# Optimization experiments

Hardware: AMD Instinct MI355X
Metric: run time of the kernel (lower is better)

The kernel has to match this reference:

```python
import jax, jax.numpy as jnp
import numpy as np

N_NODES = 100000

def gcn_conv(x, W, b, row, col, n_nodes):
    """PyG-style GCNConv: add self-loops, symmetric deg normalization,
    linear transform, scatter-add aggregation over edges, plus bias."""
    h = x @ W  # [N, out]
    loop = jnp.arange(n_nodes, dtype=row.dtype)
    r = jnp.concatenate([row, loop])  # source nodes
    c = jnp.concatenate([col, loop])  # target nodes
    w = jnp.ones(r.shape[0], dtype=x.dtype)  # edge_weight=None -> ones (incl. self-loop fill=1)
    deg = jax.ops.segment_sum(w, c, num_segments=n_nodes)
    dinv = jnp.where(deg > 0, jax.lax.rsqrt(deg), 0.0).astype(x.dtype)
    norm = dinv[r] * dinv[c]  # [E+N]
    msg = h[r] * norm[:, None]  # gather + scale, [E+N, out]
    out = jax.ops.segment_sum(msg, c, num_segments=n_nodes)
    return out + b


def setup_inputs() -> dict:
    key = jax.random.key(0)
    k0, k1, k2, k3, k4, k5 = jax.random.split(key, 6)
    F_in, H, C = 128, 64, 40
    E = 1_600_000
    x = jax.random.normal(k0, (N_NODES, F_in), dtype=jnp.float32)
    edge_index = jax.random.randint(k1, (2, E), 0, N_NODES, dtype=jnp.int64 if jax.config.jax_enable_x64 else jnp.int32)
    # Glorot init like torch Linear
    s1 = 1.0 / np.sqrt(F_in)
    s2 = 1.0 / np.sqrt(H)
    W1 = jax.random.uniform(k2, (F_in, H), jnp.float32, -s1, s1)
    b1 = jax.random.uniform(k3, (H,), jnp.float32, -s1, s1)
    W2 = jax.random.uniform(k4, (H, C), jnp.float32, -s2, s2)
    b2 = jax.random.uniform(k5, (C,), jnp.float32, -s2, s2)
    return {"x": x, "edge_index": edge_index, "W1": W1, "b1": b1, "W2": W2, "b2": b2}


def reference(x, edge_index, W1, b1, W2, b2):
    row, col = edge_index[0], edge_index[1]
    # eval mode: dropout(p=0.5, training=False) is identity
    h = gcn_conv(x, W1, b1, row, col, N_NODES)
    h = jax.nn.relu(h)
    out = gcn_conv(h, W2, b2, row, col, N_NODES)
    return out
```

## Files before the change

kernel.cpp:

```cpp
#include <hip/hip_runtime.h>
#include <hip/hip_fp16.h>


#define FIN 128
#define H1  64
#define C2  40
#define GP  64
#define TILE 8192
#define BCAP 6144

__global__ __launch_bounds__(256) void k_hist(const int* __restrict__ col, int E,
                                              int* __restrict__ bucketCnt, int NB) {
    __shared__ int lh[512];
    int t = threadIdx.x;
    for (int i = t; i < NB; i += 256) lh[i] = 0;
    __syncthreads();
    int base = blockIdx.x * TILE;
    int cnt = min(TILE, E - base);
    for (int i = t; i < cnt; i += 256) atomicAdd(&lh[col[base + i] >> 8], 1);
    __syncthreads();
    for (int b = t; b < NB; b += 256) if (lh[b]) atomicAdd(&bucketCnt[b], lh[b]);
}

__global__ __launch_bounds__(512) void k_scan(const int* __restrict__ bucketCnt,
                                              int* __restrict__ rawBase,
                                              int* __restrict__ padBase,
                                              int* __restrict__ gcursor,
                                              __half* __restrict__ h1,
                                              __half* __restrict__ g,
                                              int NB, int N) {
    __shared__ int sr[512], sp[512];
    int t = threadIdx.x;
    int c = (t < NB) ? bucketCnt[t] : 0;
    int p = (t < NB) ? (((c + 3) & ~3) + 1024) : 0;
    sr[t] = c; sp[t] = p;
    __syncthreads();
    for (int off = 1; off < 512; off <<= 1) {
        int a = (t >= off) ? sr[t - off] : 0;
        int b = (t >= off) ? sp[t - off] : 0;
        __syncthreads();
        sr[t] += a; sp[t] += b;
        __syncthreads();
    }
    if (t <= NB) {
        rawBase[t] = sr[t] - ((t < NB) ? c : 0);
        padBase[t] = sp[t] - ((t < NB) ? p : 0);
        if (t < NB) gcursor[t] = sr[t] - c;
    }
    if (t < 32) ((unsigned*)(h1 + (size_t)N * H1))[t] = 0u;
    else if (t < 64) ((unsigned*)(g + (size_t)N * GP))[t - 32] = 0u;
}

__global__ __launch_bounds__(512) void k_scatter(const int* __restrict__ row,
                                                 const int* __restrict__ col,
                                                 int* __restrict__ gcursor,
                                                 int* __restrict__ pairs,
                                                 int E, int NB) {
    __shared__ int2 stage[TILE];
    __shared__ int lcnt[512];
    __shared__ int lex[512];
    __shared__ int gbase[512];
    int t = threadIdx.x, tile = blockIdx.x;
    int base = tile * TILE;
    int cnt = min(TILE, E - base);

    lcnt[t] = 0;
    __syncthreads();
    for (int i = t; i < cnt; i += 512) atomicAdd(&lcnt[col[base + i] >> 8], 1);
    __syncthreads();

    int myc = lcnt[t];
    lex[t] = myc;
    __syncthreads();
    for (int off = 1; off < 512; off <<= 1) {
        int u = (t >= off) ? lex[t - off] : 0;
        __syncthreads();
        lex[t] += u;
        __syncthreads();
    }
    int ex = lex[t] - myc;
    __syncthreads();
    lex[t] = ex;
    lcnt[t] = ex;
    if (t < NB && myc > 0) gbase[t] = atomicAdd(&gcursor[t], myc);
    __syncthreads();

    for (int i = t; i < cnt; i += 512) {
        int r = row[base + i], c = col[base + i];
        int lpos = atomicAdd(&lcnt[c >> 8], 1);
        stage[lpos] = make_int2(r, c);
    }
    __syncthreads();

    for (int i = t; i < cnt; i += 512) {
        int2 p = stage[i];
        int b = p.y >> 8;
        pairs[gbase[b] + (i - lex[b])] = p.x | ((p.y & 255) << 24);
    }
}

__global__ __launch_bounds__(512) void k_bucket(const int* __restrict__ pairs,
                                                const int* __restrict__ rawBase,
                                                const int* __restrict__ padBase,
                                                int* __restrict__ rowptr,
                                                int* __restrict__ deg,
                                                int* __restrict__ esrc,
                                                int N, int NB) {
    __shared__ int dcnt[256];
    __shared__ int sr[256], sp[256];
    __shared__ int cur[256];
    __shared__ int outbuf[BCAP];
    int t = threadIdx.x, b = blockIdx.x;
    int d0 = b << 8;
    int nd = min(256, N - d0);
    int bstart = rawBase[b];
    int cnt = rawBase[b + 1] - bstart;
    int pstart = padBase[b];

    if (t < 256) dcnt[t] = 0;
    __syncthreads();
    for (int i = t; i < cnt; i += 512) {
        unsigned p = (unsigned)pairs[bstart + i];
        atomicAdd(&dcnt[p >> 24], 1);
    }
    __syncthreads();

    int myc = 0, myp = 0;
    if (t < 256) {
        myc = dcnt[t];
        myp = (myc + 3) & ~3;
        sr[t] = myc; sp[t] = myp;
    }
    __syncthreads();
    for (int off = 1; off < 256; off <<= 1) {
        int a = 0, c2 = 0;
        if (t < 256 && t >= off) { a = sr[t - off]; c2 = sp[t - off]; }
        __syncthreads();
        if (t < 256) { sr[t] += a; sp[t] += c2; }
        __syncthreads();
    }
    if (t < 256) {
        int pex = sp[t] - myp;
        cur[t] = pex;
        if (t < nd) {
            rowptr[d0 + t] = pstart + pex;
            deg[d0 + t] = myc;
        }
    }
    __syncthreads();
    int pcnt = sp[255];

    if (pcnt <= BCAP) {
        for (int i = t; i < cnt; i += 512) {
            unsigned p = (unsigned)pairs[bstart + i];
            int lpos = atomicAdd(&cur[p >> 24], 1);
            outbuf[lpos] = (int)(p & 0xFFFFFF);
        }
        __syncthreads();
        if (t < 256) {
            int pex = sp[t] - myp;
            for (int j = myc; j < myp; ++j) outbuf[pex + j] = N;
        }
        __syncthreads();
        for (int i = t; i < pcnt; i += 512) esrc[pstart + i] = outbuf[i];
    } else {
        for (int i = t; i < cnt; i += 512) {
            unsigned p = (unsigned)pairs[bstart + i];
            int lpos = atomicAdd(&cur[p >> 24], 1);
            esrc[pstart + lpos] = (int)(p & 0xFFFFFF);
        }
        __syncthreads();
        if (t < 256) {
            int pex = sp[t] - myp;
            for (int j = myc; j < myp; ++j) esrc[pstart + pex + j] = N;
        }
    }
}

__global__ __launch_bounds__(256) void k_gemm1(const float* __restrict__ x,
                                               const float* __restrict__ W1,
                                               const int* __restrict__ deg,
                                               __half* __restrict__ h1, int N) {
    __shared__ float smem[FIN * H1 + 64 * (FIN + 4)];
    __shared__ float sdc[64];
    int t = threadIdx.x;
    float* Ws = smem;
    float (*xs)[FIN + 4] = (float (*)[FIN + 4])(smem + FIN * H1);
    int node0 = blockIdx.x * 64;

    const float4* W4 = (const float4*)W1;
    float4* Ws4 = (float4*)Ws;
#pragma unroll
    for (int j = 0; j < 8; ++j) Ws4[t + j * 256] = W4[t + j * 256];

    const float4* x4 = (const float4*)x;
#pragma unroll
    for (int j = 0; j < 8; ++j) {
        int idx = t + j * 256;
        int r = idx >> 5, kq = idx & 31;
        int node = node0 + r; if (node >= N) node = N - 1;
        float4 v = x4[(size_t)node * 32 + kq];
        *(float4*)&xs[r][kq * 4] = v;
    }
    if (t < 64) {
        int node = node0 + t;
        sdc[t] = (node < N) ? rsqrtf((float)deg[node] + 1.0f) : 0.f;
    }
    __syncthreads();

    int og = t & 15, ng = t >> 4;
    int o0 = og * 4, n0 = ng * 4;
    float acc[4][4];
#pragma unroll
    for (int i = 0; i < 4; ++i)
#pragma unroll
        for (int j = 0; j < 4; ++j) acc[i][j] = 0.f;

#pragma unroll 8
    for (int k = 0; k < FIN; ++k) {
        float a0 = xs[n0 + 0][k], a1 = xs[n0 + 1][k];
        float a2 = xs[n0 + 2][k], a3 = xs[n0 + 3][k];
        float4 w = *(const float4*)&Ws[k * H1 + o0];
        acc[0][0] += a0 * w.x; acc[0][1] += a0 * w.y; acc[0][2] += a0 * w.z; acc[0][3] += a0 * w.w;
        acc[1][0] += a1 * w.x; acc[1][1] += a1 * w.y; acc[1][2] += a1 * w.z; acc[1][3] += a1 * w.w;
        acc[2][0] += a2 * w.x; acc[2][1] += a2 * w.y; acc[2][2] += a2 * w.z; acc[2][3] += a2 * w.w;
        acc[3][0] += a3 * w.x; acc[3][1] += a3 * w.y; acc[3][2] += a3 * w.z; acc[3][3] += a3 * w.w;
    }

#pragma unroll
    for (int i = 0; i < 4; ++i) {
        int node = node0 + n0 + i;
        if (node < N) {
            float dcv = sdc[n0 + i];
            union { __half h[4]; uint2 u; } pk;
            pk.h[0] = __float2half_rn(acc[i][0] * dcv);
            pk.h[1] = __float2half_rn(acc[i][1] * dcv);
            pk.h[2] = __float2half_rn(acc[i][2] * dcv);
            pk.h[3] = __float2half_rn(acc[i][3] * dcv);
            *(uint2*)&h1[(size_t)node * H1 + o0] = pk.u;
        }
    }
}

__global__ __launch_bounds__(512) void k_agg1mm(const int* __restrict__ rowptr,
                                                const int* __restrict__ deg,
                                                const int* __restrict__ esrc,
                                                const __half* __restrict__ h1,
                                                const float* __restrict__ b1,
                                                const float* __restrict__ W2,
                                                __half* __restrict__ g, int N) {
    __shared__ float hs[64][H1 + 4];
    __shared__ float Ws[H1 * C2];
    __shared__ float sdc[64];
    int t = threadIdx.x;
    int node0 = blockIdx.x * 64;

    {
        const float4* W4 = (const float4*)W2;
        float4* Ws4 = (float4*)Ws;
        for (int i = t; i < 640; i += 512) Ws4[i] = W4[i];
    }

    int wv = t >> 6, lane = t & 63;
    int half = lane >> 5;
    int f = lane & 31;
    float2 b1v = *(const float2*)&b1[2 * f];
    const __half2* hp = (const __half2*)h1;

    for (int j = 0; j < 8; ++j) {
        int r = wv * 8 + j;
        int node = node0 + r;
        if (node >= N) {
            if (lane < 32) { hs[r][2 * f] = 0.f; hs[r][2 * f + 1] = 0.f; }
            if (lane == 0) sdc[r] = 0.f;
            continue;
        }
        int start = rowptr[node], d = deg[node];
        int d4 = (d + 3) & ~3;
        float dc = rsqrtf((float)d + 1.0f);
        float ax = 0.f, ay = 0.f;
        int i = 0;
        for (; i + 8 <= d4; i += 8) {
            int4 s = *(const int4*)&esrc[start + i + half * 4];
            float2 v0 = __half22float2(hp[s.x * 32 + f]);
            float2 v1 = __half22float2(hp[s.y * 32 + f]);
            float2 v2 = __half22float2(hp[s.z * 32 + f]);
            float2 v3 = __half22float2(hp[s.w * 32 + f]);
            ax += (v0.x + v1.x) + (v2.x + v3.x);
            ay += (v0.y + v1.y) + (v2.y + v3.y);
        }
        if (i < d4 && half == 0) {
            int4 s = *(const int4*)&esrc[start + i];
            float2 v0 = __half22float2(hp[s.x * 32 + f]);
            float2 v1 = __half22float2(hp[s.y * 32 + f]);
            float2 v2 = __half22float2(hp[s.z * 32 + f]);
            float2 v3 = __half22float2(hp[s.w * 32 + f]);
            ax += (v0.x + v1.x) + (v2.x + v3.x);
            ay += (v0.y + v1.y) + (v2.y + v3.y);
        }
        ax += __shfl(ax, lane ^ 32);
        ay += __shfl(ay, lane ^ 32);
        float2 sv = __half22float2(hp[node * 32 + f]);
        ax = fmaxf(fmaf(dc, ax + sv.x, b1v.x), 0.f);
        ay = fmaxf(fmaf(dc, ay + sv.y, b1v.y), 0.f);
        if (lane < 32) { hs[r][2 * f] = ax; hs[r][2 * f + 1] = ay; }
        if (lane == 0) sdc[r] = dc;
    }
    __syncthreads();

    int og = t & 15, ng = t >> 4;
    int o0 = og * 4, n0 = ng * 2;
    int o0c = (o0 <= 36) ? o0 : 36;
    float acc[2][4];
#pragma unroll
    for (int i = 0; i < 2; ++i)
#pragma unroll
        for (int j = 0; j < 4; ++j) acc[i][j] = 0.f;

#pragma unroll 8
    for (int k = 0; k < H1; ++k) {
        float a0 = hs[n0 + 0][k], a1 = hs[n0 + 1][k];
        float4 w = *(const float4*)&Ws[k * C2 + o0c];
        acc[0][0] += a0 * w.x; acc[0][1] += a0 * w.y; acc[0][2] += a0 * w.z; acc[0][3] += a0 * w.w;
        acc[1][0] += a1 * w.x; acc[1][1] += a1 * w.y; acc[1][2] += a1 * w.z; acc[1][3] += a1 * w.w;
    }

    if (o0 < C2) {
#pragma unroll
        for (int i = 0; i < 2; ++i) {
            int node = node0 + n0 + i;
            if (node < N) {
                float dcv = sdc[n0 + i];
                union { __half h[4]; uint2 u; } pk;
                pk.h[0] = __float2half_rn(acc[i][0] * dcv);
                pk.h[1] = __float2half_rn(acc[i][1] * dcv);
                pk.h[2] = __float2half_rn(acc[i][2] * dcv);
                pk.h[3] = __float2half_rn(acc[i][3] * dcv);
                *(uint2*)&g[(size_t)node * GP + o0] = pk.u;
            }
        }
    }
}

__global__ __launch_bounds__(256) void k_agg2(const int* __restrict__ rowptr,
                                              const int* __restrict__ deg,
                                              const int* __restrict__ esrc,
                                              const __half* __restrict__ g,
                                              const float* __restrict__ b2,
                                              float* __restrict__ out, int N) {
    int w = (int)((blockIdx.x * blockDim.x + threadIdx.x) >> 6);
    int lane = threadIdx.x & 63;
    if (w >= N) return;
    int half = lane >> 5;
    int f = lane & 31;
    bool act = f < 20;
    const __half2* gp = (const __half2*)g;

    int start = rowptr[w], d = deg[w];
    int d4 = (d + 3) & ~3;
    float dc = rsqrtf((float)d + 1.0f);
    float ax = 0.f, ay = 0.f;
    int i = 0;
    for (; i + 8 <= d4; i += 8) {
        int4 s = *(const int4*)&esrc[start + i + half * 4];
        float2 v0 = __half22float2(gp[s.x * 32 + f]);
        float2 v1 = __half22float2(gp[s.y * 32 + f]);
        float2 v2 = __half22float2(gp[s.z * 32 + f]);
        float2 v3 = __half22float2(gp[s.w * 32 + f]);
        ax += (v0.x + v1.x) + (v2.x + v3.x);
        ay += (v0.y + v1.y) + (v2.y + v3.y);
    }
    if (i < d4 && half == 0) {
        int4 s = *(const int4*)&esrc[start + i];
        float2 v0 = __half22float2(gp[s.x * 32 + f]);
        float2 v1 = __half22float2(gp[s.y * 32 + f]);
        float2 v2 = __half22float2(gp[s.z * 32 + f]);
        float2 v3 = __half22float2(gp[s.w * 32 + f]);
        ax += (v0.x + v1.x) + (v2.x + v3.x);
        ay += (v0.y + v1.y) + (v2.y + v3.y);
    }
    ax += __shfl(ax, lane ^ 32);
    ay += __shfl(ay, lane ^ 32);
    if (lane < 32 && act) {
        float2 b2v = *(const float2*)&b2[2 * f];
        float2 sv = __half22float2(gp[w * 32 + f]);
        float2 o;
        o.x = fmaf(dc, ax + sv.x, b2v.x);
        o.y = fmaf(dc, ay + sv.y, b2v.y);
        *(float2*)&out[(size_t)w * C2 + 2 * f] = o;
    }
}

extern "C" void kernel_launch(void* const* d_in, const int* in_sizes, int n_in,
                              void* d_out, int out_size, void* d_ws, size_t ws_size,
                              hipStream_t stream) {
    const float* x   = (const float*)d_in[0];
    const int*   ei  = (const int*)d_in[1];
    const float* W1  = (const float*)d_in[2];
    const float* b1  = (const float*)d_in[3];
    const float* W2  = (const float*)d_in[4];
    const float* b2  = (const float*)d_in[5];
    float* out = (float*)d_out;

    const int N = in_sizes[0] / FIN;
    const int E = in_sizes[1] / 2;
    const int* row = ei;
    const int* col = ei + E;

    const int NB = (N + 255) >> 8;
    const int T  = (E + TILE - 1) / TILE;
    const int EP = E + NB * 1024 + 1024;

    char* ws = (char*)d_ws;
    size_t off = 0;
    int*    bucketCnt = (int*)(ws + off);    off += (size_t)NB * 4;
    int*    rawBase   = (int*)(ws + off);    off += (size_t)(NB + 1) * 4;
    int*    padBase   = (int*)(ws + off);    off += (size_t)(NB + 1) * 4;
    int*    gcursor   = (int*)(ws + off);    off += (size_t)NB * 4;
    int*    deg       = (int*)(ws + off);    off += (size_t)N * 4;
    int*    rowptr    = (int*)(ws + off);    off += (size_t)N * 4;
    int*    pairs     = (int*)(ws + off);    off += (size_t)E * 4;
    off = (off + 15) & ~(size_t)15;
    int*    esrc      = (int*)(ws + off);    off += (size_t)EP * 4;
    off = (off + 15) & ~(size_t)15;
    __half* h1        = (__half*)(ws + off); off += (size_t)(N + 1) * H1 * 2;
    off = (off + 15) & ~(size_t)15;
    __half* g         = (__half*)(ws + off); off += (size_t)(N + 1) * GP * 2;

    hipMemsetAsync(bucketCnt, 0, (size_t)NB * 4, stream);

    int gblocks = (N + 63) / 64;

    k_hist<<<T, 256, 0, stream>>>(col, E, bucketCnt, NB);
    k_scan<<<1, 512, 0, stream>>>(bucketCnt, rawBase, padBase, gcursor, h1, g, NB, N);
    k_scatter<<<T, 512, 0, stream>>>(row, col, gcursor, pairs, E, NB);
    k_bucket<<<NB, 512, 0, stream>>>(pairs, rawBase, padBase, rowptr, deg, esrc, N, NB);

    k_gemm1<<<gblocks, 256, 0, stream>>>(x, W1, deg, h1, N);

    k_agg1mm<<<gblocks, 512, 0, stream>>>(rowptr, deg, esrc, h1, b1, W2, g, N);

    k_agg2<<<((size_t)N * 64 + 255) / 256, 256, 0, stream>>>(rowptr, deg, esrc, g, b2, out, N);
}
```

Measured before the change: 260.4 us.

## Use split-fp16 MFMA for first GEMM and widen gather unroll to eight

The first linear layer moves from scalar FP32 FMAs to MFMA 16x16x16 fp16 instructions. Both x and a transposed W1 are split into hi/lo fp16 parts, and three MFMAs per tile keep accuracy close to FP32. The W1 split is precomputed in the scan kernel. CSR padding goes from 4 to 8 and both aggregation kernels gather eight neighbours per half-wave per iteration to raise memory-level parallelism, at the cost of more padding entries. The second GEMM reads activations as float4, and BCAP is increased.

```diff
diff --git a/kernel.cpp b/kernel.cpp
--- a/kernel.cpp
+++ b/kernel.cpp
@@ -7,7 +7,11 @@
 #define C2  40
 #define GP  64
 #define TILE 8192
-#define BCAP 6144
+#define BCAP 7168
+#define WTS 132
+
+typedef _Float16 half4_t __attribute__((ext_vector_type(4)));
+typedef float float4_t __attribute__((ext_vector_type(4)));
 
 __global__ __launch_bounds__(256) void k_hist(const int* __restrict__ col, int E,
                                               int* __restrict__ bucketCnt, int NB) {
@@ -28,11 +32,14 @@
                                               int* __restrict__ gcursor,
                                               __half* __restrict__ h1,
                                               __half* __restrict__ g,
+                                              const float* __restrict__ W1,
+                                              _Float16* __restrict__ W1th,
+                                              _Float16* __restrict__ W1tl,
                                               int NB, int N) {
     __shared__ int sr[512], sp[512];
     int t = threadIdx.x;
     int c = (t < NB) ? bucketCnt[t] : 0;
-    int p = (t < NB) ? (((c + 3) & ~3) + 1024) : 0;
+    int p = (t < NB) ? (((c + 7) & ~7) + 2048) : 0;
     sr[t] = c; sp[t] = p;
     __syncthreads();
     for (int off = 1; off < 512; off <<= 1) {
@@ -49,6 +56,13 @@
     }
     if (t < 32) ((unsigned*)(h1 + (size_t)N * H1))[t] = 0u;
     else if (t < 64) ((unsigned*)(g + (size_t)N * GP))[t - 32] = 0u;
+    for (int i = t; i < FIN * H1; i += 512) {
+        int o = i >> 7, k = i & 127;
+        float wv = W1[k * H1 + o];
+        _Float16 hi = (_Float16)wv;
+        W1th[o * WTS + k] = hi;
+        W1tl[o * WTS + k] = (_Float16)(wv - (float)hi);
+    }
 }
 
 __global__ __launch_bounds__(512) void k_scatter(const int* __restrict__ row,
@@ -128,7 +142,7 @@
     int myc = 0, myp = 0;
     if (t < 256) {
         myc = dcnt[t];
-        myp = (myc + 3) & ~3;
+        myp = (myc + 7) & ~7;
         sr[t] = myc; sp[t] = myp;
     }
     __syncthreads();
@@ -177,67 +191,68 @@
     }
 }
 
-__global__ __launch_bounds__(256) void k_gemm1(const float* __restrict__ x,
-                                               const float* __restrict__ W1,
-                                               const int* __restrict__ deg,
-                                               __half* __restrict__ h1, int N) {
-    __shared__ float smem[FIN * H1 + 64 * (FIN + 4)];
-    __shared__ float sdc[64];
+__global__ __launch_bounds__(256) void k_gemm1m(const float* __restrict__ x,
+                                                const _Float16* __restrict__ W1th,
+                                                const _Float16* __restrict__ W1tl,
+                                                const int* __restrict__ deg,
+                                                __half* __restrict__ h1, int N) {
+    __shared__ alignas(16) _Float16 Wh[H1 * WTS];
+    __shared__ alignas(16) _Float16 Wl[H1 * WTS];
     int t = threadIdx.x;
-    float* Ws = smem;
-    float (*xs)[FIN + 4] = (float (*)[FIN + 4])(smem + FIN * H1);
-    int node0 = blockIdx.x * 64;
-
-    const float4* W4 = (const float4*)W1;
-    float4* Ws4 = (float4*)Ws;
-#pragma unroll
-    for (int j = 0; j < 8; ++j) Ws4[t + j * 256] = W4[t + j * 256];
-
-    const float4* x4 = (const float4*)x;
-#pragma unroll
-    for (int j = 0; j < 8; ++j) {
-        int idx = t + j * 256;
-        int r = idx >> 5, kq = idx & 31;
-        int node = node0 + r; if (node >= N) node = N - 1;
-        float4 v = x4[(size_t)node * 32 + kq];
-        *(float4*)&xs[r][kq * 4] = v;
-    }
-    if (t < 64) {
-        int node = node0 + t;
-        sdc[t] = (node < N) ? rsqrtf((float)deg[node] + 1.0f) : 0.f;
-    }
-    __syncthreads();
-
-    int og = t & 15, ng = t >> 4;
-    int o0 = og * 4, n0 = ng * 4;
-    float acc[4][4];
-#pragma unroll
-    for (int i = 0; i < 4; ++i)
-#pragma unroll
-        for (int j = 0; j < 4; ++j) acc[i][j] = 0.f;
-
-#pragma unroll 8
-    for (int k = 0; k < FIN; ++k) {
-        float a0 = xs[n0 + 0][k], a1 = xs[n0 + 1][k];
-        float a2 = xs[n0 + 2][k], a3 = xs[n0 + 3][k];
-        float4 w = *(const float4*)&Ws[k * H1 + o0];
-        acc[0][0] += a0 * w.x; acc[0][1] += a0 * w.y; acc[0][2] += a0 * w.z; acc[0][3] += a0 * w.w;
-        acc[1][0] += a1 * w.x; acc[1][1] += a1 * w.y; acc[1][2] += a1 * w.z; acc[1][3] += a1 * w.w;
-        acc[2][0] += a2 * w.x; acc[2][1] += a2 * w.y; acc[2][2] += a2 * w.z; acc[2][3] += a2 * w.w;
-        acc[3][0] += a3 * w.x; acc[3][1] += a3 * w.y; acc[3][2] += a3 * w.z; acc[3][3] += a3 * w.w;
-    }
-
-#pragma unroll
-    for (int i = 0; i < 4; ++i) {
-        int node = node0 + n0 + i;
-        if (node < N) {
-            float dcv = sdc[n0 + i];
+
+    {
+        const uint4* sh = (const uint4*)W1th;
+        const uint4* sl = (const uint4*)W1tl;
+        uint4* dh = (uint4*)Wh;
+        uint4* dl = (uint4*)Wl;
+        for (int i = t; i < (H1 * WTS) / 8; i += 256) { dh[i] = sh[i]; dl[i] = sl[i]; }
+    }
+
+    int wv = t >> 6, l = t & 63;
+    int col = l & 15;
+    int krow = l >> 4;
+    int node = blockIdx.x * 64 + wv * 16 + col;
+    int nodec = min(node, N - 1);
+
+    half4_t bh[8], bl[8];
+    const float4* xr = (const float4*)(x + (size_t)nodec * FIN);
+#pragma unroll
+    for (int kt = 0; kt < 8; ++kt) {
+        float4 v = xr[kt * 4 + krow];
+        half4_t hi, lo;
+        hi[0] = (_Float16)v.x; lo[0] = (_Float16)(v.x - (float)hi[0]);
+        hi[1] = (_Float16)v.y; lo[1] = (_Float16)(v.y - (float)hi[1]);
+        hi[2] = (_Float16)v.z; lo[2] = (_Float16)(v.z - (float)hi[2]);
+        hi[3] = (_Float16)v.w; lo[3] = (_Float16)(v.w - (float)hi[3]);
+        bh[kt] = hi; bl[kt] = lo;
+    }
+    float dcv = rsqrtf((float)deg[nodec] + 1.0f);
+    __syncthreads();
+
+    float4_t acc[4];
+#pragma unroll
+    for (int ot = 0; ot < 4; ++ot) acc[ot] = (float4_t){0.f, 0.f, 0.f, 0.f};
+
+#pragma unroll
+    for (int kt = 0; kt < 8; ++kt) {
+#pragma unroll
+        for (int ot = 0; ot < 4; ++ot) {
+            int aoff = ((ot * 16 + col) * WTS + kt * 16 + krow * 4) >> 2;
+            half4_t ah = ((const half4_t*)Wh)[aoff];
+            half4_t al = ((const half4_t*)Wl)[aoff];
+            acc[ot] = __builtin_amdgcn_mfma_f32_16x16x16f16(ah, bh[kt], acc[ot], 0, 0, 0);
+            acc[ot] = __builtin_amdgcn_mfma_f32_16x16x16f16(ah, bl[kt], acc[ot], 0, 0, 0);
+            acc[ot] = __builtin_amdgcn_mfma_f32_16x16x16f16(al, bh[kt], acc[ot], 0, 0, 0);
+        }
+    }
+
+    if (node < N) {
+#pragma unroll
+        for (int ot = 0; ot < 4; ++ot) {
             union { __half h[4]; uint2 u; } pk;
-            pk.h[0] = __float2half_rn(acc[i][0] * dcv);
-            pk.h[1] = __float2half_rn(acc[i][1] * dcv);
-            pk.h[2] = __float2half_rn(acc[i][2] * dcv);
-            pk.h[3] = __float2half_rn(acc[i][3] * dcv);
-            *(uint2*)&h1[(size_t)node * H1 + o0] = pk.u;
+#pragma unroll
+            for (int r = 0; r < 4; ++r) pk.h[r] = __float2half_rn(acc[ot][r] * dcv);
+            *(uint2*)&h1[(size_t)node * H1 + ot * 16 + krow * 4] = pk.u;
         }
     }
 }
@@ -276,11 +291,26 @@
             continue;
         }
         int start = rowptr[node], d = deg[node];
-        int d4 = (d + 3) & ~3;
+        int d8 = (d + 7) & ~7;
         float dc = rsqrtf((float)d + 1.0f);
         float ax = 0.f, ay = 0.f;
         int i = 0;
-        for (; i + 8 <= d4; i += 8) {
+        for (; i + 16 <= d8; i += 16) {
+            int b0 = start + i + half * 8;
+            int4 sA = *(const int4*)&esrc[b0];
+            int4 sB = *(const int4*)&esrc[b0 + 4];
+            float2 v0 = __half22float2(hp[sA.x * 32 + f]);
+            float2 v1 = __half22float2(hp[sA.y * 32 + f]);
+            float2 v2 = __half22float2(hp[sA.z * 32 + f]);
+            float2 v3 = __half22float2(hp[sA.w * 32 + f]);
+            float2 v4 = __half22float2(hp[sB.x * 32 + f]);
+            float2 v5 = __half22float2(hp[sB.y * 32 + f]);
+            float2 v6 = __half22float2(hp[sB.z * 32 + f]);
+            float2 v7 = __half22float2(hp[sB.w * 32 + f]);
+            ax += ((v0.x + v1.x) + (v2.x + v3.x)) + ((v4.x + v5.x) + (v6.x + v7.x));
+            ay += ((v0.y + v1.y) + (v2.y + v3.y)) + ((v4.y + v5.y) + (v6.y + v7.y));
+        }
+        if (i < d8) {
             int4 s = *(const int4*)&esrc[start + i + half * 4];
             float2 v0 = __half22float2(hp[s.x * 32 + f]);
             float2 v1 = __half22float2(hp[s.y * 32 + f]);
@@ -289,15 +319,6 @@
             ax += (v0.x + v1.x) + (v2.x + v3.x);
             ay += (v0.y + v1.y) + (v2.y + v3.y);
         }
-        if (i < d4 && half == 0) {
-            int4 s = *(const int4*)&esrc[start + i];
-            float2 v0 = __half22float2(hp[s.x * 32 + f]);
-            float2 v1 = __half22float2(hp[s.y * 32 + f]);
-            float2 v2 = __half22float2(hp[s.z * 32 + f]);
-            float2 v3 = __half22float2(hp[s.w * 32 + f]);
-            ax += (v0.x + v1.x) + (v2.x + v3.x);
-            ay += (v0.y + v1.y) + (v2.y + v3.y);
-        }
         ax += __shfl(ax, lane ^ 32);
         ay += __shfl(ay, lane ^ 32);
         float2 sv = __half22float2(hp[node * 32 + f]);
@@ -317,12 +338,20 @@
 #pragma unroll
         for (int j = 0; j < 4; ++j) acc[i][j] = 0.f;
 
-#pragma unroll 8
-    for (int k = 0; k < H1; ++k) {
-        float a0 = hs[n0 + 0][k], a1 = hs[n0 + 1][k];
-        float4 w = *(const float4*)&Ws[k * C2 + o0c];
-        acc[0][0] += a0 * w.x; acc[0][1] += a0 * w.y; acc[0][2] += a0 * w.z; acc[0][3] += a0 * w.w;
-        acc[1][0] += a1 * w.x; acc[1][1] += a1 * w.y; acc[1][2] += a1 * w.z; acc[1][3] += a1 * w.w;
+#pragma unroll
+    for (int k = 0; k < H1; k += 4) {
+        float4 a0 = *(const float4*)&hs[n0 + 0][k];
+        float4 a1 = *(const float4*)&hs[n0 + 1][k];
+        float ar0[4] = {a0.x, a0.y, a0.z, a0.w};
+        float ar1[4] = {a1.x, a1.y, a1.z, a1.w};
+#pragma unroll
+        for (int kk = 0; kk < 4; ++kk) {
+            float4 w = *(const float4*)&Ws[(k + kk) * C2 + o0c];
+            acc[0][0] += ar0[kk] * w.x; acc[0][1] += ar0[kk] * w.y;
+            acc[0][2] += ar0[kk] * w.z; acc[0][3] += ar0[kk] * w.w;
+            acc[1][0] += ar1[kk] * w.x; acc[1][1] += ar1[kk] * w.y;
+            acc[1][2] += ar1[kk] * w.z; acc[1][3] += ar1[kk] * w.w;
+        }
     }
 
     if (o0 < C2) {
@@ -357,21 +386,27 @@
     const __half2* gp = (const __half2*)g;
 
     int start = rowptr[w], d = deg[w];
-    int d4 = (d + 3) & ~3;
+    int d8 = (d + 7) & ~7;
     float dc = rsqrtf((float)d + 1.0f);
     float ax = 0.f, ay = 0.f;
     int i = 0;
-    for (; i + 8 <= d4; i += 8) {
+    for (; i + 16 <= d8; i += 16) {
+        int b0 = start + i + half * 8;
+        int4 sA = *(const int4*)&esrc[b0];
+        int4 sB = *(const int4*)&esrc[b0 + 4];
+        float2 v0 = __half22float2(gp[sA.x * 32 + f]);
+        float2 v1 = __half22float2(gp[sA.y * 32 + f]);
+        float2 v2 = __half22float2(gp[sA.z * 32 + f]);
+        float2 v3 = __half22float2(gp[sA.w * 32 + f]);
+        float2 v4 = __half22float2(gp[sB.x * 32 + f]);
+        float2 v5 = __half22float2(gp[sB.y * 32 + f]);
+        float2 v6 = __half22float2(gp[sB.z * 32 + f]);
+        float2 v7 = __half22float2(gp[sB.w * 32 + f]);
+        ax += ((v0.x + v1.x) + (v2.x + v3.x)) + ((v4.x + v5.x) + (v6.x + v7.x));
+        ay += ((v0.y + v1.y) + (v2.y + v3.y)) + ((v4.y + v5.y) + (v6.y + v7.y));
+    }
+    if (i < d8) {
         int4 s = *(const int4*)&esrc[start + i + half * 4];
-        float2 v0 = __half22float2(gp[s.x * 32 + f]);
-        float2 v1 = __half22float2(gp[s.y * 32 + f]);
-        float2 v2 = __half22float2(gp[s.z * 32 + f]);
-        float2 v3 = __half22float2(gp[s.w * 32 + f]);
-        ax += (v0.x + v1.x) + (v2.x + v3.x);
-        ay += (v0.y + v1.y) + (v2.y + v3.y);
-    }
-    if (i < d4 && half == 0) {
-        int4 s = *(const int4*)&esrc[start + i];
         float2 v0 = __half22float2(gp[s.x * 32 + f]);
         float2 v1 = __half22float2(gp[s.y * 32 + f]);
         float2 v2 = __half22float2(gp[s.z * 32 + f]);
@@ -409,7 +444,7 @@
 
     const int NB = (N + 255) >> 8;
     const int T  = (E + TILE - 1) / TILE;
-    const int EP = E + NB * 1024 + 1024;
+    const int EP = E + NB * 2048 + 1024;
 
     char* ws = (char*)d_ws;
     size_t off = 0;
@@ -423,6 +458,10 @@
     off = (off + 15) & ~(size_t)15;
     int*    esrc      = (int*)(ws + off);    off += (size_t)EP * 4;
     off = (off + 15) & ~(size_t)15;
+    _Float16* W1th    = (_Float16*)(ws + off); off += (size_t)H1 * WTS * 2;
+    off = (off + 15) & ~(size_t)15;
+    _Float16* W1tl    = (_Float16*)(ws + off); off += (size_t)H1 * WTS * 2;
+    off = (off + 15) & ~(size_t)15;
     __half* h1        = (__half*)(ws + off); off += (size_t)(N + 1) * H1 * 2;
     off = (off + 15) & ~(size_t)15;
     __half* g         = (__half*)(ws + off); off += (size_t)(N + 1) * GP * 2;
@@ -432,11 +471,12 @@
     int gblocks = (N + 63) / 64;
 
     k_hist<<<T, 256, 0, stream>>>(col, E, bucketCnt, NB);
-    k_scan<<<1, 512, 0, stream>>>(bucketCnt, rawBase, padBase, gcursor, h1, g, NB, N);
+    k_scan<<<1, 512, 0, stream>>>(bucketCnt, rawBase, padBase, gcursor, h1, g,
+                                  W1, W1th, W1tl, NB, N);
     k_scatter<<<T, 512, 0, stream>>>(row, col, gcursor, pairs, E, NB);
     k_bucket<<<NB, 512, 0, stream>>>(pairs, rawBase, padBase, rowptr, deg, esrc, N, NB);
 
-    k_gemm1<<<gblocks, 256, 0, stream>>>(x, W1, deg, h1, N);
+    k_gemm1m<<<gblocks, 256, 0, stream>>>(x, W1th, W1tl, deg, h1, N);
 
     k_agg1mm<<<gblocks, 512, 0, stream>>>(rowptr, deg, esrc, h1, b1, W2, g, N);
 
```

Result: slower. 467.5 us (+79.6%).
